# Optimization experiments

Hardware: AMD Instinct MI355X
Metric: run time of the kernel (lower is better)

## Reference

```python
import jax, jax.numpy as jnp
import numpy as np
from jax import lax

B, IMG, PATCH, INNER = 8, 224, 16, 4
EMB, MLP_DEPTH, DEPTH, HEADS = 512, 3, 24, 8
Hp = Wp = IMG // PATCH            # 14
N = Hp * Wp                       # 196
D4, D8 = EMB // 4, EMB // 2       # 128, 256
RPE_L = (2 * Hp - 1) * (2 * Wp - 1)  # 729
EPS = 1e-5


def _ln(x, g, b):
    m = jnp.mean(x, -1, keepdims=True)
    v = jnp.mean(jnp.square(x - m), -1, keepdims=True)
    return (x - m) * lax.rsqrt(v + EPS) * g + b


def _mlp(x, w1, b1, w2, b2):
    return jax.nn.gelu(x @ w1 + b1, approximate=False) @ w2 + b2


def _merge(x, ng, nb, rw):
    # merge 2x2 inner patches: dim -> 4*dim, then project to 2*dim
    x = jnp.concatenate([x[..., 0::2, 0::2, :], x[..., 1::2, 0::2, :],
                         x[..., 0::2, 1::2, :], x[..., 1::2, 1::2, :]], axis=-1)
    return _ln(x, ng, nb) @ rw


def _rpe_index():
    coords = np.stack(np.meshgrid(np.arange(Hp), np.arange(Wp), indexing='ij')).reshape(2, -1)
    rel = (coords[:, :, None] - coords[:, None, :]).transpose(1, 2, 0).astype(np.int64)
    rel[:, :, 0] += Hp - 1
    rel[:, :, 1] += Wp - 1
    rel[:, :, 0] *= 2 * Wp - 1
    return jnp.asarray(rel.sum(-1), dtype=jnp.int32)  # [N, N]


def setup_inputs():
    key = jax.random.key(0)
    cnt = [0]
    def rnd(shape, s=0.02):
        cnt[0] += 1
        return jax.random.normal(jax.random.fold_in(key, cnt[0]), shape, jnp.float32) * s
    d = {}
    d['image'] = jax.random.normal(jax.random.fold_in(key, 999), (B, 3, IMG, IMG), jnp.float32)
    d['conv_w'] = rnd((D4, 3, 4, 4)); d['conv_b'] = jnp.zeros((D4,), jnp.float32)
    d['pn_g'] = jnp.ones((D4,), jnp.float32); d['pn_b'] = jnp.zeros((D4,), jnp.float32)
    for pre, dim in (('s1', D4), ('s2', D8)):
        h = dim * 3  # bridge_mlp_ratio = 3
        d[pre + '_ng'] = jnp.ones((MLP_DEPTH, dim), jnp.float32)
        d[pre + '_nb'] = jnp.zeros((MLP_DEPTH, dim), jnp.float32)
        d[pre + '_w1'] = rnd((MLP_DEPTH, dim, h)); d[pre + '_b1'] = jnp.zeros((MLP_DEPTH, h), jnp.float32)
        d[pre + '_w2'] = rnd((MLP_DEPTH, h, dim)); d[pre + '_b2'] = jnp.zeros((MLP_DEPTH, dim), jnp.float32)
    d['pm1_ng'] = jnp.ones((4 * D4,), jnp.float32); d['pm1_nb'] = jnp.zeros((4 * D4,), jnp.float32); d['pm1_rw'] = rnd((4 * D4, 2 * D4))
    d['pm2_ng'] = jnp.ones((4 * D8,), jnp.float32); d['pm2_nb'] = jnp.zeros((4 * D8,), jnp.float32); d['pm2_rw'] = rnd((4 * D8, 2 * D8))
    d['ape'] = rnd((1, N, EMB))
    d['mb_n1g'] = jnp.ones((DEPTH, EMB), jnp.float32); d['mb_n1b'] = jnp.zeros((DEPTH, EMB), jnp.float32)
    d['mb_qkvw'] = rnd((DEPTH, EMB, 3 * EMB)); d['mb_qkvb'] = jnp.zeros((DEPTH, 3 * EMB), jnp.float32)
    d['mb_tab'] = rnd((DEPTH, RPE_L, HEADS))
    d['mb_projw'] = rnd((DEPTH, EMB, EMB)); d['mb_projb'] = jnp.zeros((DEPTH, EMB), jnp.float32)
    d['mb_n2g'] = jnp.ones((DEPTH, EMB), jnp.float32); d['mb_n2b'] = jnp.zeros((DEPTH, EMB), jnp.float32)
    d['mb_w1'] = rnd((DEPTH, EMB, 4 * EMB)); d['mb_b1'] = jnp.zeros((DEPTH, 4 * EMB), jnp.float32)
    d['mb_w2'] = rnd((DEPTH, 4 * EMB, EMB)); d['mb_b2'] = jnp.zeros((DEPTH, EMB), jnp.float32)
    d['rpe_index'] = _rpe_index()
    return d


def _forward(image, conv_w, conv_b, pn_g, pn_b,
             s1_ng, s1_nb, s1_w1, s1_b1, s1_w2, s1_b2,
             pm1_ng, pm1_nb, pm1_rw,
             s2_ng, s2_nb, s2_w1, s2_b1, s2_w2, s2_b2,
             pm2_ng, pm2_nb, pm2_rw, ape,
             mb_n1g, mb_n1b, mb_qkvw, mb_qkvb, mb_tab, mb_projw, mb_projb,
             mb_n2g, mb_n2b, mb_w1, mb_b1, mb_w2, mb_b2, rpe_index):
    # PatchEmbed: 4x4/4 conv then split into 16x16 patches of 4x4 inner patches
    x = lax.conv_general_dilated(image, conv_w, (4, 4), 'VALID',
                                 dimension_numbers=('NCHW', 'OIHW', 'NCHW'))
    x = x + conv_b[None, :, None, None]                       # [B, D4, 56, 56]
    b = x.shape[0]
    x = x.reshape(b, D4, Hp, INNER, Wp, INNER).transpose(0, 2, 4, 3, 5, 1)
    x = x.reshape(b, N, INNER, INNER, D4)
    x = _ln(x, pn_g, pn_b)

    def mlp_step(h, p):
        ng, nb, w1, b1, w2, b2 = p
        return h + _mlp(_ln(h, ng, nb), w1, b1, w2, b2), None

    x, _ = lax.scan(mlp_step, x, (s1_ng, s1_nb, s1_w1, s1_b1, s1_w2, s1_b2))
    x = _merge(x, pm1_ng, pm1_nb, pm1_rw)                     # inner 2x2, dim 256
    x, _ = lax.scan(mlp_step, x, (s2_ng, s2_nb, s2_w1, s2_b1, s2_w2, s2_b2))
    x = _merge(x, pm2_ng, pm2_nb, pm2_rw)                     # inner 1x1, dim 512
    x = x.reshape(b, N, EMB) + ape                            # absolute pos embed

    hd = EMB // HEADS
    scale = hd ** -0.5
    f32 = jnp.finfo(jnp.float32)

    def attn_step(h, p):
        n1g, n1b, qw, qb, tab, pw, pb, n2g, n2b, w1, b1, w2, b2 = p
        y = _ln(h, n1g, n1b)
        qkv = (y @ qw + qb).reshape(b, N, 3, HEADS, hd).transpose(2, 0, 3, 1, 4)
        q, k, v = qkv[0] * scale, qkv[1], qkv[2]
        bias = tab[rpe_index].transpose(2, 0, 1)              # [H, N, N] rpe gather
        a = jnp.einsum('bhqd,bhkd->bhqk', q, k) + bias[None]
        a = jnp.clip(a.astype(jnp.float32), f32.min, f32.max)
        a = jax.nn.softmax(a, axis=-1).astype(h.dtype)
        y = jnp.einsum('bhqk,bhkd->bhqd', a, v).transpose(0, 2, 1, 3).reshape(b, N, EMB)
        h = h + (y @ pw + pb)
        h = h + _mlp(_ln(h, n2g, n2b), w1, b1, w2, b2)
        return h, None

    x, _ = lax.scan(attn_step, x, (mb_n1g, mb_n1b, mb_qkvw, mb_qkvb, mb_tab,
                                   mb_projw, mb_projb, mb_n2g, mb_n2b,
                                   mb_w1, mb_b1, mb_w2, mb_b2))
    return x


def reference(image, conv_w, conv_b, pn_g, pn_b,
              s1_ng, s1_nb, s1_w1, s1_b1, s1_w2, s1_b2,
              pm1_ng, pm1_nb, pm1_rw,
              s2_ng, s2_nb, s2_w1, s2_b1, s2_w2, s2_b2,
              pm2_ng, pm2_nb, pm2_rw, ape,
              mb_n1g, mb_n1b, mb_qkvw, mb_qkvb, mb_tab, mb_projw, mb_projb,
              mb_n2g, mb_n2b, mb_w1, mb_b1, mb_w2, mb_b2, rpe_index):
    return _forward(image, conv_w, conv_b, pn_g, pn_b,
                    s1_ng, s1_nb, s1_w1, s1_b1, s1_w2, s1_b2,
                    pm1_ng, pm1_nb, pm1_rw,
                    s2_ng, s2_nb, s2_w1, s2_b1, s2_w2, s2_b2,
                    pm2_ng, pm2_nb, pm2_rw, ape,
                    mb_n1g, mb_n1b, mb_qkvw, mb_qkvb, mb_tab, mb_projw, mb_projb,
                    mb_n2g, mb_n2b, mb_w1, mb_b1, mb_w2, mb_b2, rpe_index)
```

## Files before the change

kernel.cpp:

```cpp
#include <hip/hip_runtime.h>
#include <hip/hip_bf16.h>

#define Bb    8
#define IMG   224
#define Hp    14
#define Np    196
#define D4    128
#define D8    256
#define EMB   512
#define HEADS 8
#define RPEL  729
#define DEPTH 24
#define EPS   1e-5f

constexpr int EPI_NONE = 0, EPI_BIAS = 1, EPI_BIAS_GELU = 2, EPI_BIAS_RES = 3, EPI_ATOMIC = 4;

typedef __bf16 bf16x8 __attribute__((ext_vector_type(8)));
typedef float  f32x4  __attribute__((ext_vector_type(4)));

static __device__ __forceinline__ void gload16(const void* g, void* l) {
    __builtin_amdgcn_global_load_lds(
        (const __attribute__((address_space(1))) void*)g,
        (__attribute__((address_space(3))) void*)l, 16, 0, 0);
}

__global__ __launch_bounds__(128) void conv_ln_kernel(
    const float* __restrict__ img, const float* __restrict__ cw,
    const float* __restrict__ cb,  const float* __restrict__ png,
    const float* __restrict__ pnb, float* __restrict__ xout)
{
    int p = blockIdx.x;
    int b = p / 3136, rem = p % 3136;
    int hh = rem / 56, ww = rem % 56;
    __shared__ float win[48];
    __shared__ float red[4];
    int t = threadIdx.x;
    if (t < 48) {
        int ic = t >> 4, kh = (t >> 2) & 3, kw = t & 3;
        win[t] = img[(((size_t)b*3 + ic)*224 + hh*4 + kh)*224 + ww*4 + kw];
    }
    __syncthreads();
    float acc = cb[t];
    const float* wrow = cw + (size_t)t * 48;
    #pragma unroll
    for (int r = 0; r < 48; ++r) acc += win[r] * wrow[r];
    float s = acc, ss = acc * acc;
    #pragma unroll
    for (int o = 32; o > 0; o >>= 1) { s += __shfl_xor(s, o, 64); ss += __shfl_xor(ss, o, 64); }
    int wv = t >> 6;
    if ((t & 63) == 0) { red[wv*2] = s; red[wv*2+1] = ss; }
    __syncthreads();
    s = red[0] + red[2]; ss = red[1] + red[3];
    float mean = s * (1.f/128.f);
    float rstd = rsqrtf(ss * (1.f/128.f) - mean*mean + EPS);
    float v = (acc - mean) * rstd * png[t] + pnb[t];
    int hp = hh >> 2, ih = hh & 3, wp = ww >> 2, iw = ww & 3;
    int bn = b * Np + hp * Hp + wp;
    xout[((size_t)bn*16 + ih*4 + iw)*128 + t] = v;
}

__global__ __launch_bounds__(256) void ln_kernel(
    const float* __restrict__ x, const float* __restrict__ g,
    const float* __restrict__ b, __bf16* __restrict__ y, int M, int D)
{
    int wave = threadIdx.x >> 6, lane = threadIdx.x & 63;
    int row = blockIdx.x * 4 + wave;
    if (row >= M) return;
    const float* xr = x + (size_t)row * D;
    float s = 0.f, ss = 0.f;
    for (int i = lane; i < D; i += 64) { float v = xr[i]; s += v; ss += v*v; }
    #pragma unroll
    for (int o = 32; o > 0; o >>= 1) { s += __shfl_xor(s, o, 64); ss += __shfl_xor(ss, o, 64); }
    float inv = 1.f / (float)D;
    float mean = s * inv;
    float rstd = rsqrtf(ss * inv - mean*mean + EPS);
    __bf16* yr = y + (size_t)row * D;
    for (int i = lane; i < D; i += 64)
        yr[i] = (__bf16)((xr[i] - mean) * rstd * g[i] + b[i]);
}

__global__ __launch_bounds__(256) void merge1_ln_kernel(
    const float* __restrict__ x, const float* __restrict__ g,
    const float* __restrict__ b, __bf16* __restrict__ y)
{
    int wave = threadIdx.x >> 6, lane = threadIdx.x & 63;
    int row = blockIdx.x * 4 + wave;
    if (row >= 6272) return;
    int j2 = row & 1, i2 = (row >> 1) & 1, bn = row >> 2;
    float vals[8]; float s = 0.f, ss = 0.f;
    #pragma unroll
    for (int t = 0; t < 8; ++t) {
        int e = lane + t*64;
        int k = e >> 7, c = e & 127;
        int ih = 2*i2 + (k & 1), iw = 2*j2 + (k >> 1);
        float v = x[((size_t)bn*16 + ih*4 + iw)*128 + c];
        vals[t] = v; s += v; ss += v*v;
    }
    #pragma unroll
    for (int o = 32; o > 0; o >>= 1) { s += __shfl_xor(s, o, 64); ss += __shfl_xor(ss, o, 64); }
    float mean = s * (1.f/512.f);
    float rstd = rsqrtf(ss * (1.f/512.f) - mean*mean + EPS);
    __bf16* yr = y + (size_t)row * 512;
    #pragma unroll
    for (int t = 0; t < 8; ++t) {
        int e = lane + t*64;
        yr[e] = (__bf16)((vals[t] - mean) * rstd * g[e] + b[e]);
    }
}

__global__ __launch_bounds__(256) void merge2_ln_kernel(
    const float* __restrict__ x, const float* __restrict__ g,
    const float* __restrict__ b, __bf16* __restrict__ y)
{
    int wave = threadIdx.x >> 6, lane = threadIdx.x & 63;
    int row = blockIdx.x * 4 + wave;
    if (row >= 1568) return;
    float vals[16]; float s = 0.f, ss = 0.f;
    #pragma unroll
    for (int t = 0; t < 16; ++t) {
        int e = lane + t*64;
        int k = e >> 8, c = e & 255;
        float v = x[((size_t)row*4 + (k & 1)*2 + (k >> 1))*256 + c];
        vals[t] = v; s += v; ss += v*v;
    }
    #pragma unroll
    for (int o = 32; o > 0; o >>= 1) { s += __shfl_xor(s, o, 64); ss += __shfl_xor(ss, o, 64); }
    float mean = s * (1.f/1024.f);
    float rstd = rsqrtf(ss * (1.f/1024.f) - mean*mean + EPS);
    __bf16* yr = y + (size_t)row * 1024;
    #pragma unroll
    for (int t = 0; t < 16; ++t) {
        int e = lane + t*64;
        yr[e] = (__bf16)((vals[t] - mean) * rstd * g[e] + b[e]);
    }
}

static __device__ __forceinline__ void tconv_tile(
    const float* __restrict__ in, __bf16* __restrict__ out,
    int R, int C, int tile, float (*t)[33])
{
    int tiles_c = C >> 5;
    int tr = tile / tiles_c, tc = tile - tr * tiles_c;
    int ty = threadIdx.x >> 3, tx = threadIdx.x & 7;
    const float4 v = *(const float4*)&in[(size_t)(tr*32 + ty) * C + (tc*32 + tx*4)];
    t[ty][tx*4+0] = v.x; t[ty][tx*4+1] = v.y; t[ty][tx*4+2] = v.z; t[ty][tx*4+3] = v.w;
    __syncthreads();
    __bf16 o[4];
    #pragma unroll
    for (int j = 0; j < 4; ++j) o[j] = (__bf16)t[tx*4+j][ty];
    *(uint2*)&out[(size_t)(tc*32 + ty) * R + (tr*32 + tx*4)] = *(const uint2*)o;
}

__global__ __launch_bounds__(256) void tconv_kernel(
    const float* __restrict__ in, __bf16* __restrict__ out, int R, int C)
{
    __shared__ float t[32][33];
    size_t off = (size_t)blockIdx.y * R * C;
    tconv_tile(in + off, out + off, R, C, blockIdx.x, t);
}

__global__ __launch_bounds__(256) void layer_tconv_kernel(
    const float* __restrict__ qkvw, const float* __restrict__ projw,
    const float* __restrict__ w1, const float* __restrict__ w2,
    __bf16* __restrict__ LW)
{
    __shared__ float t[32][33];
    int b = blockIdx.x;
    if (b < 768)        tconv_tile(qkvw,  LW,           512, 1536, b,        t);
    else if (b < 1024)  tconv_tile(projw, LW +  786432, 512,  512, b -  768, t);
    else if (b < 2048)  tconv_tile(w1,    LW + 1048576, 512, 2048, b - 1024, t);
    else                tconv_tile(w2,    LW + 2097152, 2048, 512, b - 2048, t);
}

template<int BM, int EPI>
__global__ __launch_bounds__(256) void gemm_kernel(
    const __bf16* __restrict__ A, const __bf16* __restrict__ Bt,
    const float* __restrict__ bias, const float* __restrict__ Rres,
    void* __restrict__ Cv, int M, int N, int K, int kChunk)
{
    constexpr int BF = (BM == 128) ? 4 : 2;
    __shared__ __bf16 As[BM][32];
    __shared__ __bf16 Bs[128][32];
    const int tid = threadIdx.x, lane = tid & 63, wave = tid >> 6;
    const int m0 = blockIdx.y * BM, n0 = blockIdx.x << 7;
    int wm, wn;
    if constexpr (BM == 128) { wm = (wave >> 1) << 6; wn = (wave & 1) << 6; }
    else                     { wm = 0;                wn = wave << 5;       }
    const int q = lane >> 4, mr = lane & 15;
    const int kstart = blockIdx.z * kChunk;
    const int kend   = min(kstart + kChunk, K);

    f32x4 acc[4][BF];
    #pragma unroll
    for (int i = 0; i < 4; ++i)
        #pragma unroll
        for (int j = 0; j < BF; ++j)
            acc[i][j] = (f32x4){0.f, 0.f, 0.f, 0.f};

    const int crow = tid >> 2, ccol = (tid & 3) << 3;
    const __bf16* ag0 = A + (size_t)min(m0 + crow, M - 1) * K + ccol;
    const __bf16* ag1 = ag0;
    if constexpr (BM == 128)
        ag1 = A + (size_t)min(m0 + 64 + crow, M - 1) * K + ccol;
    const __bf16* bg0 = Bt + (size_t)(n0 + crow) * K + ccol;
    const __bf16* bg1 = Bt + (size_t)(n0 + 64 + crow) * K + ccol;
    char* lA = (char*)&As[0][0] + wave * 1024;
    char* lB = (char*)&Bs[0][0] + wave * 1024;

    for (int k0 = kstart; k0 < kend; k0 += 32) {
        gload16(ag0 + k0, lA);
        if constexpr (BM == 128) gload16(ag1 + k0, lA + 4096);
        gload16(bg0 + k0, lB);
        gload16(bg1 + k0, lB + 4096);
        __syncthreads();
        bf16x8 af[4], bfr[BF];
        #pragma unroll
        for (int i = 0; i < 4; ++i)
            af[i] = *(const bf16x8*)&As[wm + i*16 + mr][q*8];
        #pragma unroll
        for (int j = 0; j < BF; ++j)
            bfr[j] = *(const bf16x8*)&Bs[wn + j*16 + mr][q*8];
        #pragma unroll
        for (int i = 0; i < 4; ++i)
            #pragma unroll
            for (int j = 0; j < BF; ++j)
                acc[i][j] = __builtin_amdgcn_mfma_f32_16x16x32_bf16(af[i], bfr[j], acc[i][j], 0, 0, 0);
        __syncthreads();
    }

    const bool addb = (blockIdx.z == 0);
    #pragma unroll
    for (int i = 0; i < 4; ++i) {
        #pragma unroll
        for (int j = 0; j < BF; ++j) {
            const int n = n0 + wn + j*16 + mr;
            float bv = 0.f;
            if constexpr (EPI != EPI_NONE) bv = bias[n];
            #pragma unroll
            for (int r = 0; r < 4; ++r) {
                const int m = m0 + wm + i*16 + q*4 + r;
                if (m < M) {
                    if constexpr (EPI == EPI_ATOMIC) {
                        atomicAdd(&((float*)Cv)[(size_t)m * N + n], acc[i][j][r] + (addb ? bv : 0.f));
                    } else {
                        float v = acc[i][j][r] + bv;
                        if constexpr (EPI == EPI_BIAS_GELU)
                            v = 0.5f * v * (1.f + erff(v * 0.70710678118654752f));
                        if constexpr (EPI == EPI_BIAS_RES)
                            v += Rres[(size_t)m * N + n];
                        if constexpr (EPI == EPI_BIAS || EPI == EPI_BIAS_GELU)
                            ((__bf16*)Cv)[(size_t)m * N + n] = (__bf16)v;
                        else
                            ((float*)Cv)[(size_t)m * N + n] = v;
                    }
                }
            }
        }
    }
}

__global__ __launch_bounds__(256) void attn_kernel(
    const __bf16* __restrict__ qkv, const float* __restrict__ tab,
    const int* __restrict__ rpe, __bf16* __restrict__ y2)
{
    __shared__ __bf16 Vt[64][232];
    __shared__ __bf16 Pl[4][16][232];
    int blk = blockIdx.x;
    int qg = blk & 3, h = (blk >> 2) & 7, b = blk >> 5;
    int tid = threadIdx.x;

    for (int i = tid; i < 196*8; i += 256) {
        int key = i >> 3, seg = i & 7;
        bf16x8 v = *(const bf16x8*)(qkv + ((size_t)(b*Np + key))*1536 + 1024 + h*64 + seg*8);
        #pragma unroll
        for (int j = 0; j < 8; ++j) Vt[seg*8 + j][key] = v[j];
    }
    {
        int d0 = tid >> 2, cs = tid & 3;
        #pragma unroll
        for (int j = 0; j < 9; ++j) Vt[d0][196 + cs*9 + j] = (__bf16)0.f;
    }
    __syncthreads();

    int lane = tid & 63, wave = tid >> 6;
    int T = qg + 4*wave;
    if (T > 12) return;
    int q = lane >> 4, mr = lane & 15;

    if (lane < 36) {
        #pragma unroll
        for (int r = 0; r < 16; ++r) Pl[wave][r][196 + lane] = (__bf16)0.f;
    }

    int qtok = b*Np + min(T*16 + mr, 195);
    const __bf16* qp = qkv + (size_t)qtok*1536 + h*64 + q*8;
    bf16x8 aq0 = *(const bf16x8*)qp;
    bf16x8 aq1 = *(const bf16x8*)(qp + 32);

    f32x4 sacc[13];
    #pragma unroll
    for (int nt = 0; nt < 13; ++nt) {
        int ktok = b*Np + min(nt*16 + mr, 195);
        const __bf16* kp = qkv + (size_t)ktok*1536 + 512 + h*64 + q*8;
        bf16x8 bk0 = *(const bf16x8*)kp;
        bf16x8 bk1 = *(const bf16x8*)(kp + 32);
        f32x4 z = (f32x4){0.f, 0.f, 0.f, 0.f};
        z = __builtin_amdgcn_mfma_f32_16x16x32_bf16(aq0, bk0, z, 0, 0, 0);
        sacc[nt] = __builtin_amdgcn_mfma_f32_16x16x32_bf16(aq1, bk1, z, 0, 0, 0);
    }

    #pragma unroll
    for (int r = 0; r < 4; ++r) {
        int qi = T*16 + q*4 + r;
        const int* rrow = rpe + (size_t)min(qi, 195) * 196;
        float vals[13];
        #pragma unroll
        for (int nt = 0; nt < 13; ++nt) {
            int col = nt*16 + mr;
            float bv = tab[rrow[min(col, 195)]*8 + h];
            float v = sacc[nt][r] * 0.125f + bv;
            vals[nt] = (col < 196) ? v : -3.0e38f;
        }
        float m = vals[0];
        #pragma unroll
        for (int nt = 1; nt < 13; ++nt) m = fmaxf(m, vals[nt]);
        #pragma unroll
        for (int o = 8; o > 0; o >>= 1) m = fmaxf(m, __shfl_xor(m, o, 64));
        float s = 0.f, p[13];
        #pragma unroll
        for (int nt = 0; nt < 13; ++nt) { p[nt] = __expf(vals[nt] - m); s += p[nt]; }
        #pragma unroll
        for (int o = 8; o > 0; o >>= 1) s += __shfl_xor(s, o, 64);
        float inv = 1.f / s;
        #pragma unroll
        for (int nt = 0; nt < 13; ++nt)
            Pl[wave][q*4 + r][nt*16 + mr] = (__bf16)(p[nt] * inv);
    }

    f32x4 oacc[4];
    #pragma unroll
    for (int nt = 0; nt < 4; ++nt) oacc[nt] = (f32x4){0.f, 0.f, 0.f, 0.f};
    #pragma unroll
    for (int ks = 0; ks < 7; ++ks) {
        bf16x8 ap = *(const bf16x8*)&Pl[wave][mr][ks*32 + q*8];
        #pragma unroll
        for (int nt = 0; nt < 4; ++nt) {
            bf16x8 bv = *(const bf16x8*)&Vt[nt*16 + mr][ks*32 + q*8];
            oacc[nt] = __builtin_amdgcn_mfma_f32_16x16x32_bf16(ap, bv, oacc[nt], 0, 0, 0);
        }
    }

    #pragma unroll
    for (int nt = 0; nt < 4; ++nt) {
        #pragma unroll
        for (int r = 0; r < 4; ++r) {
            int qi = T*16 + q*4 + r;
            if (qi < 196)
                y2[((size_t)(b*Np + qi))*512 + h*64 + nt*16 + mr] = (__bf16)oacc[nt][r];
        }
    }
}

__global__ __launch_bounds__(256) void add_ape_kernel(float* __restrict__ x,
                                                      const float* __restrict__ ape)
{
    int i = blockIdx.x * 256 + threadIdx.x;
    if (i < 1568*512) x[i] += ape[i % (Np*512)];
}

extern "C" void kernel_launch(void* const* d_in, const int* in_sizes, int n_in,
                              void* d_out, int out_size, void* d_ws, size_t ws_size,
                              hipStream_t stream)
{
    typedef const float* fp;
    fp image  = (fp)d_in[0];
    fp conv_w = (fp)d_in[1];  fp conv_b = (fp)d_in[2];
    fp pn_g   = (fp)d_in[3];  fp pn_b   = (fp)d_in[4];
    fp s1_ng  = (fp)d_in[5];  fp s1_nb  = (fp)d_in[6];
    fp s1_w1  = (fp)d_in[7];  fp s1_b1  = (fp)d_in[8];
    fp s1_w2  = (fp)d_in[9];  fp s1_b2  = (fp)d_in[10];
    fp s2_ng  = (fp)d_in[11]; fp s2_nb  = (fp)d_in[12];
    fp s2_w1  = (fp)d_in[13]; fp s2_b1  = (fp)d_in[14];
    fp s2_w2  = (fp)d_in[15]; fp s2_b2  = (fp)d_in[16];
    fp pm1_ng = (fp)d_in[17]; fp pm1_nb = (fp)d_in[18]; fp pm1_rw = (fp)d_in[19];
    fp pm2_ng = (fp)d_in[20]; fp pm2_nb = (fp)d_in[21]; fp pm2_rw = (fp)d_in[22];
    fp ape    = (fp)d_in[23];
    fp n1g    = (fp)d_in[24]; fp n1b    = (fp)d_in[25];
    fp qkvw   = (fp)d_in[26]; fp qkvb   = (fp)d_in[27];
    fp tab    = (fp)d_in[28];
    fp projw  = (fp)d_in[29]; fp projb  = (fp)d_in[30];
    fp n2g    = (fp)d_in[31]; fp n2b    = (fp)d_in[32];
    fp w1     = (fp)d_in[33]; fp b1     = (fp)d_in[34];
    fp w2     = (fp)d_in[35]; fp b2     = (fp)d_in[36];
    const int* rpe = (const int*)d_in[37];

    float*  X  = (float*)d_ws;
    __bf16* H  = (__bf16*)(X + 3211264);
    __bf16* Y  = H + 9633792;
    __bf16* SW = Y + 3211264;
    __bf16* LW = SW + 2129920;

    tconv_kernel<<<dim3(48, 3),  256, 0, stream>>>(s1_w1,  SW + 0,       128, 384);
    tconv_kernel<<<dim3(48, 3),  256, 0, stream>>>(s1_w2,  SW + 147456,  384, 128);
    tconv_kernel<<<dim3(192, 3), 256, 0, stream>>>(s2_w1,  SW + 294912,  256, 768);
    tconv_kernel<<<dim3(192, 3), 256, 0, stream>>>(s2_w2,  SW + 884736,  768, 256);
    tconv_kernel<<<dim3(128, 1), 256, 0, stream>>>(pm1_rw, SW + 1474560, 512, 256);
    tconv_kernel<<<dim3(512, 1), 256, 0, stream>>>(pm2_rw, SW + 1605632, 1024, 512);

    conv_ln_kernel<<<Bb*56*56, 128, 0, stream>>>(image, conv_w, conv_b, pn_g, pn_b, X);

    for (int t = 0; t < 3; ++t) {
        ln_kernel<<<25088/4, 256, 0, stream>>>(X, s1_ng + t*128, s1_nb + t*128, Y, 25088, 128);
        gemm_kernel<128, EPI_BIAS_GELU><<<dim3(3, 196), 256, 0, stream>>>(
            Y, SW + t*49152, s1_b1 + t*384, nullptr, H, 25088, 384, 128, 128);
        gemm_kernel<64, EPI_BIAS_RES><<<dim3(1, 392), 256, 0, stream>>>(
            H, SW + 147456 + t*49152, s1_b2 + t*128, X, X, 25088, 128, 384, 384);
    }
    merge1_ln_kernel<<<6272/4, 256, 0, stream>>>(X, pm1_ng, pm1_nb, Y);
    gemm_kernel<64, EPI_NONE><<<dim3(2, 98), 256, 0, stream>>>(
        Y, SW + 1474560, nullptr, nullptr, X, 6272, 256, 512, 512);
    for (int t = 0; t < 3; ++t) {
        ln_kernel<<<6272/4, 256, 0, stream>>>(X, s2_ng + t*256, s2_nb + t*256, Y, 6272, 256);
        gemm_kernel<128, EPI_BIAS_GELU><<<dim3(6, 49), 256, 0, stream>>>(
            Y, SW + 294912 + t*196608, s2_b1 + t*768, nullptr, H, 6272, 768, 256, 256);
        gemm_kernel<64, EPI_BIAS_RES><<<dim3(2, 98), 256, 0, stream>>>(
            H, SW + 884736 + t*196608, s2_b2 + t*256, X, X, 6272, 256, 768, 768);
    }
    merge2_ln_kernel<<<1568/4, 256, 0, stream>>>(X, pm2_ng, pm2_nb, Y);
    gemm_kernel<64, EPI_NONE><<<dim3(4, 25), 256, 0, stream>>>(
        Y, SW + 1605632, nullptr, nullptr, X, 1568, 512, 1024, 1024);
    add_ape_kernel<<<(1568*512+255)/256, 256, 0, stream>>>(X, ape);

    for (int l = 0; l < DEPTH; ++l) {
        layer_tconv_kernel<<<3072, 256, 0, stream>>>(
            qkvw + (size_t)l*512*1536, projw + (size_t)l*512*512,
            w1 + (size_t)l*512*2048, w2 + (size_t)l*2048*512, LW);
        ln_kernel<<<392, 256, 0, stream>>>(X, n1g + l*EMB, n1b + l*EMB, Y, 1568, EMB);
        gemm_kernel<64, EPI_BIAS><<<dim3(12, 25), 256, 0, stream>>>(
            Y, LW, qkvb + (size_t)l*1536, nullptr, H, 1568, 1536, EMB, EMB);
        attn_kernel<<<256, 256, 0, stream>>>(H, tab + (size_t)l*RPEL*HEADS, rpe, Y);
        gemm_kernel<64, EPI_ATOMIC><<<dim3(4, 25, 4), 256, 0, stream>>>(
            Y, LW + 786432, projb + (size_t)l*EMB, nullptr, X, 1568, EMB, EMB, 128);
        ln_kernel<<<392, 256, 0, stream>>>(X, n2g + l*EMB, n2b + l*EMB, Y, 1568, EMB);
        gemm_kernel<64, EPI_BIAS_GELU><<<dim3(16, 25), 256, 0, stream>>>(
            Y, LW + 1048576, b1 + (size_t)l*2048, nullptr, H, 1568, 2048, EMB, EMB);
        gemm_kernel<64, EPI_ATOMIC><<<dim3(4, 25, 4), 256, 0, stream>>>(
            H, LW + 2097152, b2 + (size_t)l*EMB, nullptr, X, 1568, EMB, 2048, 512);
    }
    hipMemcpyAsync(d_out, X, (size_t)1568*512*sizeof(float), hipMemcpyDeviceToDevice, stream);
}
```

Measured before the change: 2.994 ms.

## Double-buffer GEMM LDS tiles and batch all-layer weight conversion upfront

```diff
diff --git a/kernel.cpp b/kernel.cpp
--- a/kernel.cpp
+++ b/kernel.cpp
@@ -162,14 +162,20 @@
 __global__ __launch_bounds__(256) void layer_tconv_kernel(
     const float* __restrict__ qkvw, const float* __restrict__ projw,
     const float* __restrict__ w1, const float* __restrict__ w2,
-    __bf16* __restrict__ LW)
+    __bf16* __restrict__ LW, size_t lw_stride)
 {
     __shared__ float t[32][33];
+    int l = blockIdx.y;
     int b = blockIdx.x;
-    if (b < 768)        tconv_tile(qkvw,  LW,           512, 1536, b,        t);
-    else if (b < 1024)  tconv_tile(projw, LW +  786432, 512,  512, b -  768, t);
-    else if (b < 2048)  tconv_tile(w1,    LW + 1048576, 512, 2048, b - 1024, t);
-    else                tconv_tile(w2,    LW + 2097152, 2048, 512, b - 2048, t);
+    const float* q_ = qkvw  + (size_t)l * 786432;
+    const float* p_ = projw + (size_t)l * 262144;
+    const float* a_ = w1    + (size_t)l * 1048576;
+    const float* c_ = w2    + (size_t)l * 1048576;
+    __bf16* o = LW + (size_t)l * lw_stride;
+    if (b < 768)        tconv_tile(q_, o,           512, 1536, b,        t);
+    else if (b < 1024)  tconv_tile(p_, o +  786432, 512,  512, b -  768, t);
+    else if (b < 2048)  tconv_tile(a_, o + 1048576, 512, 2048, b - 1024, t);
+    else                tconv_tile(c_, o + 2097152, 2048, 512, b - 2048, t);
 }
 
 template<int BM, int EPI>
@@ -178,9 +184,12 @@
     const float* __restrict__ bias, const float* __restrict__ Rres,
     void* __restrict__ Cv, int M, int N, int K, int kChunk)
 {
-    constexpr int BF = (BM == 128) ? 4 : 2;
-    __shared__ __bf16 As[BM][32];
-    __shared__ __bf16 Bs[128][32];
+    constexpr int BF  = (BM == 128) ? 4 : 2;
+    constexpr int LPT = (BM == 128) ? 4 : 3;
+    constexpr int ABYTES = BM * 64;
+    constexpr int BBYTES = 8192;
+    __shared__ __bf16 As[2][BM][32];
+    __shared__ __bf16 Bs[2][128][32];
     const int tid = threadIdx.x, lane = tid & 63, wave = tid >> 6;
     const int m0 = blockIdx.y * BM, n0 = blockIdx.x << 7;
     int wm, wn;
@@ -189,6 +198,7 @@
     const int q = lane >> 4, mr = lane & 15;
     const int kstart = blockIdx.z * kChunk;
     const int kend   = min(kstart + kChunk, K);
+    const int nt     = (kend - kstart) >> 5;
 
     f32x4 acc[4][BF];
     #pragma unroll
@@ -204,29 +214,44 @@
         ag1 = A + (size_t)min(m0 + 64 + crow, M - 1) * K + ccol;
     const __bf16* bg0 = Bt + (size_t)(n0 + crow) * K + ccol;
     const __bf16* bg1 = Bt + (size_t)(n0 + 64 + crow) * K + ccol;
-    char* lA = (char*)&As[0][0] + wave * 1024;
-    char* lB = (char*)&Bs[0][0] + wave * 1024;
-
-    for (int k0 = kstart; k0 < kend; k0 += 32) {
-        gload16(ag0 + k0, lA);
-        if constexpr (BM == 128) gload16(ag1 + k0, lA + 4096);
-        gload16(bg0 + k0, lB);
-        gload16(bg1 + k0, lB + 4096);
-        __syncthreads();
+    char* lA = (char*)&As[0][0][0] + wave * 1024;
+    char* lB = (char*)&Bs[0][0][0] + wave * 1024;
+
+#define STAGE(t_, buf_) do {                                         \
+        const int k0_ = kstart + ((t_) << 5);                        \
+        gload16(ag0 + k0_, lA + (buf_) * ABYTES);                    \
+        if constexpr (BM == 128)                                     \
+            gload16(ag1 + k0_, lA + (buf_) * ABYTES + 4096);         \
+        gload16(bg0 + k0_, lB + (buf_) * BBYTES);                    \
+        gload16(bg1 + k0_, lB + (buf_) * BBYTES + 4096);             \
+    } while (0)
+
+    STAGE(0, 0);
+    for (int t = 0; t < nt; ++t) {
+        const int cur = t & 1;
+        if (t + 1 < nt) {
+            STAGE(t + 1, cur ^ 1);
+            asm volatile("s_waitcnt vmcnt(%0)" :: "i"(LPT) : "memory");
+        } else {
+            asm volatile("s_waitcnt vmcnt(0)" ::: "memory");
+        }
+        __builtin_amdgcn_s_barrier();
         bf16x8 af[4], bfr[BF];
         #pragma unroll
         for (int i = 0; i < 4; ++i)
-            af[i] = *(const bf16x8*)&As[wm + i*16 + mr][q*8];
+            af[i] = *(const bf16x8*)&As[cur][wm + i*16 + mr][q*8];
         #pragma unroll
         for (int j = 0; j < BF; ++j)
-            bfr[j] = *(const bf16x8*)&Bs[wn + j*16 + mr][q*8];
+            bfr[j] = *(const bf16x8*)&Bs[cur][wn + j*16 + mr][q*8];
         #pragma unroll
         for (int i = 0; i < 4; ++i)
             #pragma unroll
             for (int j = 0; j < BF; ++j)
                 acc[i][j] = __builtin_amdgcn_mfma_f32_16x16x32_bf16(af[i], bfr[j], acc[i][j], 0, 0, 0);
-        __syncthreads();
-    }
+        asm volatile("s_waitcnt lgkmcnt(0)" ::: "memory");
+        __builtin_amdgcn_s_barrier();
+    }
+#undef STAGE
 
     const bool addb = (blockIdx.z == 0);
     #pragma unroll
@@ -400,12 +425,19 @@
     __bf16* SW = Y + 3211264;
     __bf16* LW = SW + 2129920;
 
+    const size_t LWSTRIDE = 3145728;
+    const size_t need_all = ((size_t)(LW - (__bf16*)d_ws)) * 2 + DEPTH * LWSTRIDE * 2;
+    const bool bigLW = ws_size >= need_all;
+
     tconv_kernel<<<dim3(48, 3),  256, 0, stream>>>(s1_w1,  SW + 0,       128, 384);
     tconv_kernel<<<dim3(48, 3),  256, 0, stream>>>(s1_w2,  SW + 147456,  384, 128);
     tconv_kernel<<<dim3(192, 3), 256, 0, stream>>>(s2_w1,  SW + 294912,  256, 768);
     tconv_kernel<<<dim3(192, 3), 256, 0, stream>>>(s2_w2,  SW + 884736,  768, 256);
     tconv_kernel<<<dim3(128, 1), 256, 0, stream>>>(pm1_rw, SW + 1474560, 512, 256);
     tconv_kernel<<<dim3(512, 1), 256, 0, stream>>>(pm2_rw, SW + 1605632, 1024, 512);
+    if (bigLW)
+        layer_tconv_kernel<<<dim3(3072, DEPTH), 256, 0, stream>>>(
+            qkvw, projw, w1, w2, LW, LWSTRIDE);
 
     conv_ln_kernel<<<Bb*56*56, 128, 0, stream>>>(image, conv_w, conv_b, pn_g, pn_b, X);
 
@@ -432,20 +464,22 @@
     add_ape_kernel<<<(1568*512+255)/256, 256, 0, stream>>>(X, ape);
 
     for (int l = 0; l < DEPTH; ++l) {
-        layer_tconv_kernel<<<3072, 256, 0, stream>>>(
-            qkvw + (size_t)l*512*1536, projw + (size_t)l*512*512,
-            w1 + (size_t)l*512*2048, w2 + (size_t)l*2048*512, LW);
+        const __bf16* LWl = bigLW ? LW + (size_t)l * LWSTRIDE : LW;
+        if (!bigLW)
+            layer_tconv_kernel<<<dim3(3072, 1), 256, 0, stream>>>(
+                qkvw + (size_t)l*512*1536, projw + (size_t)l*512*512,
+                w1 + (size_t)l*512*2048, w2 + (size_t)l*2048*512, LW, 0);
         ln_kernel<<<392, 256, 0, stream>>>(X, n1g + l*EMB, n1b + l*EMB, Y, 1568, EMB);
         gemm_kernel<64, EPI_BIAS><<<dim3(12, 25), 256, 0, stream>>>(
-            Y, LW, qkvb + (size_t)l*1536, nullptr, H, 1568, 1536, EMB, EMB);
+            Y, LWl, qkvb + (size_t)l*1536, nullptr, H, 1568, 1536, EMB, EMB);
         attn_kernel<<<256, 256, 0, stream>>>(H, tab + (size_t)l*RPEL*HEADS, rpe, Y);
         gemm_kernel<64, EPI_ATOMIC><<<dim3(4, 25, 4), 256, 0, stream>>>(
-            Y, LW + 786432, projb + (size_t)l*EMB, nullptr, X, 1568, EMB, EMB, 128);
+            Y, LWl + 786432, projb + (size_t)l*EMB, nullptr, X, 1568, EMB, EMB, 128);
         ln_kernel<<<392, 256, 0, stream>>>(X, n2g + l*EMB, n2b + l*EMB, Y, 1568, EMB);
         gemm_kernel<64, EPI_BIAS_GELU><<<dim3(16, 25), 256, 0, stream>>>(
-            Y, LW + 1048576, b1 + (size_t)l*2048, nullptr, H, 1568, 2048, EMB, EMB);
+            Y, LWl + 1048576, b1 + (size_t)l*2048, nullptr, H, 1568, 2048, EMB, EMB);
         gemm_kernel<64, EPI_ATOMIC><<<dim3(4, 25, 4), 256, 0, stream>>>(
-            H, LW + 2097152, b2 + (size_t)l*EMB, nullptr, X, 1568, EMB, 2048, 512);
+            H, LWl + 2097152, b2 + (size_t)l*EMB, nullptr, X, 1568, EMB, 2048, 512);
     }
     hipMemcpyAsync(d_out, X, (size_t)1568*512*sizeof(float), hipMemcpyDeviceToDevice, stream);
 }
```

Result: slower. 3.086 ms (+3.1%).
